# Optimization experiments

Measured on AMD Instinct MI355X. Metric: run time of the kernel, lower is better.

## Reference

```python
import jax, jax.numpy as jnp
import numpy as np

B, S = 1, 2048            # one prefill sequence, flattened to n_tokens = B*S
HID = 4096
NH, NKV, HD = 32, 8, 128  # query heads, kv heads, head dim
G, M = NKV, NH // NKV     # kv groups, query heads per group
THETA = 1e6


def setup_inputs() -> dict:
    key = jax.random.key(0)
    ks = jax.random.split(key, 5)
    h = jax.random.normal(ks[0], (B * S, HID), dtype=jnp.float32)
    position_ids = jnp.tile(jnp.arange(S, dtype=jnp.int32), B)
    wq = jax.random.normal(ks[1], (NH * HD, HID), dtype=jnp.float32) * 0.02
    wk = jax.random.normal(ks[2], (NKV * HD, HID), dtype=jnp.float32) * 0.02
    wv = jax.random.normal(ks[3], (NKV * HD, HID), dtype=jnp.float32) * 0.02
    wo = jax.random.normal(ks[4], (HID, NH * HD), dtype=jnp.float32) * 0.02
    return {"h": h, "position_ids": position_ids, "wq": wq, "wk": wk, "wv": wv, "wo": wo}


def _rope_cos_sin(position_ids):
    # non-interleaved (half-split) RoPE, default inv_freq with theta=1e6
    inv_freq = 1.0 / (THETA ** (jnp.arange(0, HD, 2, dtype=jnp.float32) / HD))  # [HD/2]
    freqs = position_ids.astype(jnp.float32)[:, None] * inv_freq[None, :]       # [n, HD/2]
    return jnp.cos(freqs)[:, None, :], jnp.sin(freqs)[:, None, :]               # broadcast over heads


def _apply_rope(x, cos, sin):
    x1, x2 = jnp.split(x, 2, axis=-1)
    return jnp.concatenate([x1 * cos - x2 * sin, x2 * cos + x1 * sin], axis=-1)


def reference(h, position_ids, wq, wk, wv, wo):
    n = h.shape[0]
    q = (h @ wq.T).reshape(n, NH, HD)
    k = (h @ wk.T).reshape(n, NKV, HD)
    v = (h @ wv.T).reshape(B, S, NKV, HD)

    cos, sin = _rope_cos_sin(position_ids)
    q = _apply_rope(q, cos, sin).reshape(B, S, G, M, HD)
    k = _apply_rope(k, cos, sin).reshape(B, S, G, HD)

    scale = 1.0 / np.sqrt(HD).astype(np.float32)
    # grouped-query attention: each kv head g serves M query heads
    scores = jnp.einsum('bqgmd,bkgd->bgmqk', q, k) * scale      # [B,G,M,S,S]
    causal = jnp.tril(jnp.ones((S, S), dtype=bool))
    scores = jnp.where(causal, scores, jnp.finfo(scores.dtype).min)
    p = jax.nn.softmax(scores, axis=-1)
    o = jnp.einsum('bgmqk,bkgd->bqgmd', p, v).reshape(n, NH * HD)
    return o @ wo.T
```

## Files before the change

kernel.cpp:

```cpp
#include <hip/hip_runtime.h>
#include <hip/hip_bf16.h>

#define S_LEN 2048
#define HID 4096
#define NH 32
#define NKV 8
#define HD 128
#define NQKV 6144

typedef unsigned short u16;
typedef unsigned int u32;
typedef __bf16 bf16x8 __attribute__((ext_vector_type(8)));
typedef float f32x4 __attribute__((ext_vector_type(4)));

__device__ __forceinline__ float bf2f(u16 u) {
    union { u32 i; float f; } x; x.i = ((u32)u) << 16; return x.f;
}
__device__ __forceinline__ u16 f2bf(float f) {
    union { float f; u32 i; } x; x.f = f;
    u32 r = x.i + 0x7fffu + ((x.i >> 16) & 1u);
    return (u16)(r >> 16);
}
__device__ __forceinline__ u32 pack2(float a, float b) {
    return (u32)f2bf(a) | ((u32)f2bf(b) << 16);
}
__device__ __forceinline__ void gld16(const u16* g, u16* l) {
    __builtin_amdgcn_global_load_lds(
        (const __attribute__((address_space(1))) u32*)g,
        (__attribute__((address_space(3))) u32*)l, 16, 0, 0);
}

__global__ __launch_bounds__(256) void cvt_f32_bf16(
    const float* __restrict__ src, u16* __restrict__ dst, int n8)
{
    int i = blockIdx.x * 256 + threadIdx.x;
    if (i >= n8) return;
    const float4* s = (const float4*)src + (size_t)i * 2;
    float4 x0 = s[0], x1 = s[1];
    uint4 p;
    p.x = pack2(x0.x, x0.y); p.y = pack2(x0.z, x0.w);
    p.z = pack2(x1.x, x1.y); p.w = pack2(x1.z, x1.w);
    *((uint4*)dst + i) = p;
}

template <bool OUTBF16>
__global__ __launch_bounds__(256) void gemm128(
    const u16* __restrict__ X, const u16* __restrict__ W,
    void* __restrict__ C, int K, int ldc)
{
    __shared__ __align__(16) u16 As[128 * 32];
    __shared__ __align__(16) u16 Bs[128 * 32];

    const int tid  = threadIdx.x;
    const int w    = tid >> 6;
    const int lane = tid & 63;
    const int quad = lane >> 4;
    const int n16  = lane & 15;

    int id = blockIdx.y * gridDim.x + blockIdx.x;
    const int nwg = gridDim.x * gridDim.y;
    if ((nwg & 7) == 0) {
        const int cpx = nwg >> 3;
        id = (id & 7) * cpx + (id >> 3);
    }
    const int m0 = (id / gridDim.x) * 128;
    const int n0 = (id % gridDim.x) * 128;

    const int wr   = (w >> 1) * 64;
    const int wc   = (w & 1) * 64;

    const int c0 = tid;
    const int c1 = tid + 256;

    f32x4 acc[4][4] = {};

    for (int k0 = 0; k0 < K; k0 += 32) {
        __syncthreads();
        gld16(X + (size_t)(m0 + (c0 >> 2)) * K + k0 + (c0 & 3) * 8,
              As + (size_t)(w * 64) * 8);
        gld16(X + (size_t)(m0 + (c1 >> 2)) * K + k0 + (c1 & 3) * 8,
              As + (size_t)(256 + w * 64) * 8);
        gld16(W + (size_t)(n0 + (c0 >> 2)) * K + k0 + (c0 & 3) * 8,
              Bs + (size_t)(w * 64) * 8);
        gld16(W + (size_t)(n0 + (c1 >> 2)) * K + k0 + (c1 & 3) * 8,
              Bs + (size_t)(256 + w * 64) * 8);
        __syncthreads();

        bf16x8 a[4], b[4];
#pragma unroll
        for (int t = 0; t < 4; ++t) {
            a[t] = *reinterpret_cast<const bf16x8*>(As + (wr + t * 16 + n16) * 32 + quad * 8);
            b[t] = *reinterpret_cast<const bf16x8*>(Bs + (wc + t * 16 + n16) * 32 + quad * 8);
        }
#pragma unroll
        for (int mt = 0; mt < 4; ++mt)
#pragma unroll
            for (int nt = 0; nt < 4; ++nt)
                acc[mt][nt] = __builtin_amdgcn_mfma_f32_16x16x32_bf16(
                    a[mt], b[nt], acc[mt][nt], 0, 0, 0);
    }

#pragma unroll
    for (int mt = 0; mt < 4; ++mt) {
        const int row0 = m0 + wr + mt * 16 + quad * 4;
#pragma unroll
        for (int nt = 0; nt < 4; ++nt) {
            const int col = n0 + wc + nt * 16 + n16;
#pragma unroll
            for (int r = 0; r < 4; ++r) {
                if constexpr (OUTBF16)
                    ((u16*)C)[(size_t)(row0 + r) * ldc + col] = f2bf(acc[mt][nt][r]);
                else
                    ((float*)C)[(size_t)(row0 + r) * ldc + col] = acc[mt][nt][r];
            }
        }
    }
}

template <bool XF32, bool OUTBF16>
__global__ __launch_bounds__(256) void gemm_bt(
    const void* __restrict__ Xv,
    const float* __restrict__ W0, int r1,
    const float* __restrict__ W1, int r2,
    const float* __restrict__ W2,
    void* __restrict__ C, int K, int ldc)
{
    __shared__ u16 Xs[64][48];
    __shared__ u16 Ws[64][48];

    const int tid  = threadIdx.x;
    const int w    = tid >> 6;
    const int lane = tid & 63;
    const int m0   = blockIdx.y * 64;
    const int n0   = blockIdx.x * 64;

    const int sr = tid >> 2;
    const int sc = (tid & 3) * 8;

    const float* xrow32 = nullptr;
    const u16*   xrow16 = nullptr;
    if constexpr (XF32) xrow32 = (const float*)Xv + (size_t)(m0 + sr) * K;
    else                xrow16 = (const u16*)Xv + (size_t)(m0 + sr) * K;

    const int wr = n0 + sr;
    const float* wrow;
    if (wr < r1)      wrow = W0 + (size_t)wr * K;
    else if (wr < r2) wrow = W1 + (size_t)(wr - r1) * K;
    else              wrow = W2 + (size_t)(wr - r2) * K;

    f32x4 acc[4] = {};
    const int mrow = w * 16 + (lane & 15);
    const int nrow = lane & 15;
    const int kq   = (lane >> 4) * 8;

    for (int k0 = 0; k0 < K; k0 += 32) {
        __syncthreads();
        if constexpr (XF32) {
            float4 x0 = *reinterpret_cast<const float4*>(xrow32 + k0 + sc);
            float4 x1 = *reinterpret_cast<const float4*>(xrow32 + k0 + sc + 4);
            uint4 p;
            p.x = pack2(x0.x, x0.y); p.y = pack2(x0.z, x0.w);
            p.z = pack2(x1.x, x1.y); p.w = pack2(x1.z, x1.w);
            *reinterpret_cast<uint4*>(&Xs[sr][sc]) = p;
        } else {
            *reinterpret_cast<uint4*>(&Xs[sr][sc]) =
                *reinterpret_cast<const uint4*>(xrow16 + k0 + sc);
        }
        {
            float4 w0v = *reinterpret_cast<const float4*>(wrow + k0 + sc);
            float4 w1v = *reinterpret_cast<const float4*>(wrow + k0 + sc + 4);
            uint4 p;
            p.x = pack2(w0v.x, w0v.y); p.y = pack2(w0v.z, w0v.w);
            p.z = pack2(w1v.x, w1v.y); p.w = pack2(w1v.z, w1v.w);
            *reinterpret_cast<uint4*>(&Ws[sr][sc]) = p;
        }
        __syncthreads();
        bf16x8 a = *reinterpret_cast<const bf16x8*>(&Xs[mrow][kq]);
#pragma unroll
        for (int t = 0; t < 4; ++t) {
            bf16x8 b = *reinterpret_cast<const bf16x8*>(&Ws[t * 16 + nrow][kq]);
            acc[t] = __builtin_amdgcn_mfma_f32_16x16x32_bf16(a, b, acc[t], 0, 0, 0);
        }
    }

    const int mb = m0 + w * 16 + ((lane >> 4) << 2);
#pragma unroll
    for (int t = 0; t < 4; ++t) {
        const int col = n0 + t * 16 + (lane & 15);
#pragma unroll
        for (int i = 0; i < 4; ++i) {
            if constexpr (OUTBF16)
                ((u16*)C)[(size_t)(mb + i) * ldc + col] = f2bf(acc[t][i]);
            else
                ((float*)C)[(size_t)(mb + i) * ldc + col] = acc[t][i];
        }
    }
}

__global__ __launch_bounds__(256) void rope_kernel(
    const u16* __restrict__ qkv, const int* __restrict__ pos,
    u16* __restrict__ qb, u16* __restrict__ kb, u16* __restrict__ vb)
{
    const int n   = blockIdx.x;
    const int tid = threadIdx.x;
    const float scale = 0.08838834764831845f;
    __shared__ float cs[64], sn[64];
    if (tid < 64) {
        float p   = (float)pos[n];
        float inv = powf(1.0e6f, -(float)tid / 64.0f);
        float f   = p * inv;
        cs[tid] = cosf(f);
        sn[tid] = sinf(f);
    }
    __syncthreads();
    const u16* row = qkv + (size_t)n * NQKV;

    for (int i = tid; i < NH * 64; i += 256) {
        int h = i >> 6, j = i & 63;
        float x1 = bf2f(row[h * HD + j]), x2 = bf2f(row[h * HD + j + 64]);
        size_t base = ((size_t)h * S_LEN + n) * HD;
        qb[base + j]      = f2bf((x1 * cs[j] - x2 * sn[j]) * scale);
        qb[base + j + 64] = f2bf((x2 * cs[j] + x1 * sn[j]) * scale);
    }
    for (int i = tid; i < NKV * 64; i += 256) {
        int g = i >> 6, j = i & 63;
        const u16* kr = row + NH * HD + g * HD;
        float x1 = bf2f(kr[j]), x2 = bf2f(kr[j + 64]);
        size_t base = ((size_t)g * S_LEN + n) * HD;
        kb[base + j]      = f2bf(x1 * cs[j] - x2 * sn[j]);
        kb[base + j + 64] = f2bf(x2 * cs[j] + x1 * sn[j]);
    }
    for (int i = tid; i < NKV * HD; i += 256) {
        int g = i >> 7, d = i & 127;
        vb[((size_t)g * S_LEN + n) * HD + d] = row[NH * HD + NKV * HD + g * HD + d];
    }
}

__global__ __launch_bounds__(256) void attn_mfma(
    const u16* __restrict__ qb, const u16* __restrict__ kb,
    const u16* __restrict__ vb, u16* __restrict__ ao)
{
    __shared__ u16 Ks[64][136];
    __shared__ u16 Vt[128][72];
    __shared__ u16 Ps[4][16][72];

    const int tid  = threadIdx.x;
    const int w    = tid >> 6;
    const int lane = tid & 63;
    const int quad = lane >> 4;
    const int n16  = lane & 15;
    const int h    = blockIdx.y;
    const int g    = h >> 2;
    const int NQT  = S_LEN / 64;

    for (int half = 0; half < 2; ++half) {
        const int qt = half ? (NQT - 1 - blockIdx.x) : blockIdx.x;
        const int q0 = qt * 64;

        bf16x8 qf[4];
        {
            const u16* qrow = qb + ((size_t)h * S_LEN + q0 + w * 16 + n16) * HD;
#pragma unroll
            for (int s = 0; s < 4; ++s)
                qf[s] = *reinterpret_cast<const bf16x8*>(qrow + s * 32 + quad * 8);
        }

        f32x4 of[8] = {};
        float mrow[4], lrow[4];
#pragma unroll
        for (int r = 0; r < 4; ++r) { mrow[r] = -1e30f; lrow[r] = 0.0f; }

        const int ntiles = qt + 1;
        for (int kt = 0; kt < ntiles; ++kt) {
            const int k0 = kt * 64;
            __syncthreads();
#pragma unroll
            for (int i = 0; i < 4; ++i) {
                int chunk = tid + 256 * i;
                int key = chunk >> 4, d0 = (chunk & 15) * 8;
                *reinterpret_cast<uint4*>(&Ks[key][d0]) =
                    *reinterpret_cast<const uint4*>(
                        kb + ((size_t)g * S_LEN + k0 + key) * HD + d0);
            }
            {
                int key = tid & 63;
                const u16* vrow = vb + ((size_t)g * S_LEN + k0 + key) * HD;
#pragma unroll
                for (int i = 0; i < 4; ++i) {
                    int d0 = (tid >> 6) * 8 + i * 32;
                    uint4 vv = *reinterpret_cast<const uint4*>(vrow + d0);
                    const u32 vw[4] = {vv.x, vv.y, vv.z, vv.w};
#pragma unroll
                    for (int t = 0; t < 4; ++t) {
                        Vt[d0 + 2 * t][key]     = (u16)(vw[t] & 0xffff);
                        Vt[d0 + 2 * t + 1][key] = (u16)(vw[t] >> 16);
                    }
                }
            }
            __syncthreads();

            f32x4 sc[4] = {};
#pragma unroll
            for (int s = 0; s < 4; ++s) {
#pragma unroll
                for (int t = 0; t < 4; ++t) {
                    bf16x8 bf = *reinterpret_cast<const bf16x8*>(
                        &Ks[t * 16 + n16][s * 32 + quad * 8]);
                    sc[t] = __builtin_amdgcn_mfma_f32_16x16x32_bf16(qf[s], bf, sc[t], 0, 0, 0);
                }
            }

            if (kt == ntiles - 1) {
                const int qbase = q0 + w * 16 + quad * 4;
#pragma unroll
                for (int t = 0; t < 4; ++t) {
                    int key = k0 + t * 16 + n16;
#pragma unroll
                    for (int r = 0; r < 4; ++r)
                        if (key > qbase + r) sc[t][r] = -1e30f;
                }
            }

#pragma unroll
            for (int r = 0; r < 4; ++r) {
                float mx = fmaxf(fmaxf(sc[0][r], sc[1][r]), fmaxf(sc[2][r], sc[3][r]));
                mx = fmaxf(mx, __shfl_xor(mx, 1));
                mx = fmaxf(mx, __shfl_xor(mx, 2));
                mx = fmaxf(mx, __shfl_xor(mx, 4));
                mx = fmaxf(mx, __shfl_xor(mx, 8));
                float mnew  = fmaxf(mrow[r], mx);
                float alpha = __expf(mrow[r] - mnew);
                float ls = 0.0f;
#pragma unroll
                for (int t = 0; t < 4; ++t) {
                    float p = __expf(sc[t][r] - mnew);
                    Ps[w][quad * 4 + r][t * 16 + n16] = f2bf(p);
                    ls += p;
                }
                ls += __shfl_xor(ls, 1);
                ls += __shfl_xor(ls, 2);
                ls += __shfl_xor(ls, 4);
                ls += __shfl_xor(ls, 8);
                lrow[r] = lrow[r] * alpha + ls;
                mrow[r] = mnew;
#pragma unroll
                for (int nt = 0; nt < 8; ++nt) of[nt][r] *= alpha;
            }
            __threadfence_block();

#pragma unroll
            for (int s = 0; s < 2; ++s) {
                bf16x8 af = *reinterpret_cast<const bf16x8*>(
                    &Ps[w][n16][s * 32 + quad * 8]);
#pragma unroll
                for (int nt = 0; nt < 8; ++nt) {
                    bf16x8 bf = *reinterpret_cast<const bf16x8*>(
                        &Vt[nt * 16 + n16][s * 32 + quad * 8]);
                    of[nt] = __builtin_amdgcn_mfma_f32_16x16x32_bf16(af, bf, of[nt], 0, 0, 0);
                }
            }
        }

#pragma unroll
        for (int r = 0; r < 4; ++r) {
            float inv = 1.0f / lrow[r];
            u16* dst = ao + (size_t)(q0 + w * 16 + quad * 4 + r) * (NH * HD) + h * HD + n16;
#pragma unroll
            for (int nt = 0; nt < 8; ++nt)
                dst[nt * 16] = f2bf(of[nt][r] * inv);
        }
    }
}

extern "C" void kernel_launch(void* const* d_in, const int* in_sizes, int n_in,
                              void* d_out, int out_size, void* d_ws, size_t ws_size,
                              hipStream_t stream)
{
    const float* h   = (const float*)d_in[0];
    const int*   pos = (const int*)d_in[1];
    const float* wq  = (const float*)d_in[2];
    const float* wk  = (const float*)d_in[3];
    const float* wv  = (const float*)d_in[4];
    const float* wo  = (const float*)d_in[5];

    char* ws = (char*)d_ws;

    if (ws_size >= 92274688ull) {
        u16* hb     = (u16*)(ws);
        u16* wqkv_b = (u16*)(ws + 16777216);
        u16* ao     = (u16*)(ws + 16777216);
        u16* kb     = (u16*)(ws + 33554432);
        u16* vb     = (u16*)(ws + 37748736);
        u16* wo_b   = (u16*)(ws + 41943040);
        u16* qkv    = (u16*)(ws + 67108864);
        u16* qb     = hb;

        cvt_f32_bf16<<<4096, 256, 0, stream>>>(h, hb, 1048576);
        cvt_f32_bf16<<<8192, 256, 0, stream>>>(wq, wqkv_b, 2097152);
        cvt_f32_bf16<<<2048, 256, 0, stream>>>(wk, wqkv_b + 16777216, 524288);
        cvt_f32_bf16<<<2048, 256, 0, stream>>>(wv, wqkv_b + 20971520, 524288);

        gemm128<true><<<dim3(NQKV / 128, S_LEN / 128), 256, 0, stream>>>(
            hb, wqkv_b, qkv, HID, NQKV);
        rope_kernel<<<S_LEN, 256, 0, stream>>>(qkv, pos, qb, kb, vb);
        cvt_f32_bf16<<<8192, 256, 0, stream>>>(wo, wo_b, 2097152);
        attn_mfma<<<dim3(S_LEN / 128, NH), 256, 0, stream>>>(qb, kb, vb, ao);
        gemm128<false><<<dim3(HID / 128, S_LEN / 128), 256, 0, stream>>>(
            ao, wo_b, d_out, NH * HD, HID);
    } else {
        u16* qkv = (u16*)(ws);
        u16* qb  = (u16*)(ws + 25165824);
        u16* kb  = (u16*)(ws + 41943040);
        u16* vb  = (u16*)(ws + 46137344);
        u16* ao  = (u16*)(ws + 50331648);

        dim3 g1(NQKV / 64, S_LEN / 64);
        gemm_bt<true, true><<<g1, 256, 0, stream>>>(
            h, wq, NH * HD, wk, NH * HD + NKV * HD, wv, qkv, HID, NQKV);
        rope_kernel<<<S_LEN, 256, 0, stream>>>(qkv, pos, qb, kb, vb);
        attn_mfma<<<dim3(S_LEN / 128, NH), 256, 0, stream>>>(qb, kb, vb, ao);
        dim3 g2(HID / 64, S_LEN / 64);
        gemm_bt<false, false><<<g2, 256, 0, stream>>>(
            ao, wo, HID, wo, HID, wo, d_out, NH * HD, HID);
    }
}
```

Baseline: 602.6 us.

## Prefetch next K/V tile into registers, swizzle LDS, alias P buffer onto K

```diff
diff --git a/kernel.cpp b/kernel.cpp
--- a/kernel.cpp
+++ b/kernel.cpp
@@ -240,9 +240,8 @@
     const u16* __restrict__ qb, const u16* __restrict__ kb,
     const u16* __restrict__ vb, u16* __restrict__ ao)
 {
-    __shared__ u16 Ks[64][136];
-    __shared__ u16 Vt[128][72];
-    __shared__ u16 Ps[4][16][72];
+    __shared__ __align__(16) u16 KPs[64 * 128];
+    __shared__ __align__(16) u16 Vt[128 * 64];
 
     const int tid  = threadIdx.x;
     const int w    = tid >> 6;
@@ -253,6 +252,10 @@
     const int g    = h >> 2;
     const int NQT  = S_LEN / 64;
 
+    const u16* kbase = kb + (size_t)g * S_LEN * HD;
+    const u16* vbase = vb + (size_t)g * S_LEN * HD;
+    const int xsw = (n16 & 7) << 3;
+
     for (int half = 0; half < 2; ++half) {
         const int qt = half ? (NQT - 1 - blockIdx.x) : blockIdx.x;
         const int q0 = qt * 64;
@@ -270,34 +273,41 @@
 #pragma unroll
         for (int r = 0; r < 4; ++r) { mrow[r] = -1e30f; lrow[r] = 0.0f; }
 
+        uint4 kreg[4], vreg[4];
+        auto load_kv = [&](int k0) {
+#pragma unroll
+            for (int i = 0; i < 4; ++i) {
+                kreg[i] = *reinterpret_cast<const uint4*>(
+                    kbase + (size_t)(k0 + (tid >> 4) + 16 * i) * HD + (tid & 15) * 8);
+                vreg[i] = *reinterpret_cast<const uint4*>(
+                    vbase + (size_t)(k0 + lane) * HD + w * 8 + i * 32);
+            }
+        };
+        load_kv(0);
+
         const int ntiles = qt + 1;
         for (int kt = 0; kt < ntiles; ++kt) {
-            const int k0 = kt * 64;
             __syncthreads();
 #pragma unroll
             for (int i = 0; i < 4; ++i) {
-                int chunk = tid + 256 * i;
-                int key = chunk >> 4, d0 = (chunk & 15) * 8;
-                *reinterpret_cast<uint4*>(&Ks[key][d0]) =
-                    *reinterpret_cast<const uint4*>(
-                        kb + ((size_t)g * S_LEN + k0 + key) * HD + d0);
-            }
-            {
-                int key = tid & 63;
-                const u16* vrow = vb + ((size_t)g * S_LEN + k0 + key) * HD;
-#pragma unroll
-                for (int i = 0; i < 4; ++i) {
-                    int d0 = (tid >> 6) * 8 + i * 32;
-                    uint4 vv = *reinterpret_cast<const uint4*>(vrow + d0);
-                    const u32 vw[4] = {vv.x, vv.y, vv.z, vv.w};
-#pragma unroll
-                    for (int t = 0; t < 4; ++t) {
-                        Vt[d0 + 2 * t][key]     = (u16)(vw[t] & 0xffff);
-                        Vt[d0 + 2 * t + 1][key] = (u16)(vw[t] >> 16);
-                    }
+                const int key = (tid >> 4) + 16 * i;
+                const int d0  = (tid & 15) * 8;
+                *reinterpret_cast<uint4*>(
+                    &KPs[key * 128 + (d0 ^ ((key & 7) << 3))]) = kreg[i];
+            }
+#pragma unroll
+            for (int i = 0; i < 4; ++i) {
+                const int d0 = w * 8 + i * 32;
+                const u32 vw[4] = {vreg[i].x, vreg[i].y, vreg[i].z, vreg[i].w};
+#pragma unroll
+                for (int t = 0; t < 4; ++t) {
+                    const int r0 = d0 + 2 * t;
+                    Vt[r0 * 64 + (lane ^ ((r0 & 7) << 3))]             = (u16)(vw[t] & 0xffff);
+                    Vt[(r0 + 1) * 64 + (lane ^ (((r0 + 1) & 7) << 3))] = (u16)(vw[t] >> 16);
                 }
             }
             __syncthreads();
+            if (kt + 1 < ntiles) load_kv((kt + 1) * 64);
 
             f32x4 sc[4] = {};
 #pragma unroll
@@ -305,7 +315,7 @@
 #pragma unroll
                 for (int t = 0; t < 4; ++t) {
                     bf16x8 bf = *reinterpret_cast<const bf16x8*>(
-                        &Ks[t * 16 + n16][s * 32 + quad * 8]);
+                        &KPs[(t * 16 + n16) * 128 + ((s * 32 + quad * 8) ^ xsw)]);
                     sc[t] = __builtin_amdgcn_mfma_f32_16x16x32_bf16(qf[s], bf, sc[t], 0, 0, 0);
                 }
             }
@@ -314,12 +324,14 @@
                 const int qbase = q0 + w * 16 + quad * 4;
 #pragma unroll
                 for (int t = 0; t < 4; ++t) {
-                    int key = k0 + t * 16 + n16;
+                    int key = kt * 64 + t * 16 + n16;
 #pragma unroll
                     for (int r = 0; r < 4; ++r)
                         if (key > qbase + r) sc[t][r] = -1e30f;
                 }
             }
+
+            __syncthreads();
 
 #pragma unroll
             for (int r = 0; r < 4; ++r) {
@@ -331,10 +343,11 @@
                 float mnew  = fmaxf(mrow[r], mx);
                 float alpha = __expf(mrow[r] - mnew);
                 float ls = 0.0f;
+                const int pr = quad * 4 + r;
 #pragma unroll
                 for (int t = 0; t < 4; ++t) {
                     float p = __expf(sc[t][r] - mnew);
-                    Ps[w][quad * 4 + r][t * 16 + n16] = f2bf(p);
+                    KPs[(w * 16 + pr) * 64 + ((t * 16 + n16) ^ ((pr & 7) << 3))] = f2bf(p);
                     ls += p;
                 }
                 ls += __shfl_xor(ls, 1);
@@ -351,11 +364,11 @@
 #pragma unroll
             for (int s = 0; s < 2; ++s) {
                 bf16x8 af = *reinterpret_cast<const bf16x8*>(
-                    &Ps[w][n16][s * 32 + quad * 8]);
+                    &KPs[(w * 16 + n16) * 64 + ((s * 32 + quad * 8) ^ xsw)]);
 #pragma unroll
                 for (int nt = 0; nt < 8; ++nt) {
                     bf16x8 bf = *reinterpret_cast<const bf16x8*>(
-                        &Vt[nt * 16 + n16][s * 32 + quad * 8]);
+                        &Vt[(nt * 16 + n16) * 64 + ((s * 32 + quad * 8) ^ xsw)]);
                     of[nt] = __builtin_amdgcn_mfma_f32_16x16x32_bf16(af, bf, of[nt], 0, 0, 0);
                 }
             }
```

Result: faster. 581.4 us (-3.5%).
